# Kernel optimization log

Hardware: AMD Instinct MI355X
Metric: run time of the kernel (lower is better)

Reference implementation:

```python
import jax, jax.numpy as jnp
import numpy as np

EPS = 1e-10   # eps added inside cumprod, as in _compute_weights
FAR = 1e10    # last delta, as in forward()
NEAR_D, FAR_D = 2.0, 6.0  # typical NeRF near/far bounds for depth sampling

N_RAYS, N_PTS = 65536, 128


def setup_inputs() -> dict:
    key = jax.random.key(0)
    k1, k2, k3 = jax.random.split(key, 3)
    # densities are non-negative (raw sigma output after relu/softplus)
    density = jax.random.uniform(k1, (N_RAYS, N_PTS), dtype=jnp.float32) * 2.0
    feature = jax.random.uniform(k2, (N_RAYS, N_PTS, 3), dtype=jnp.float32)
    # monotonically increasing sample depths along each ray in [NEAR_D, FAR_D]
    depth_values = jnp.sort(
        jax.random.uniform(k3, (N_RAYS, N_PTS), dtype=jnp.float32,
                           minval=NEAR_D, maxval=FAR_D), axis=-1)
    return {"density": density, "feature": feature, "depth_values": depth_values}


def reference(density, feature, depth_values):
    # deltas: diff of sample depths, last delta = 1e10  -> [N, P]
    deltas = jnp.concatenate(
        [depth_values[..., 1:] - depth_values[..., :-1],
         jnp.full_like(depth_values[..., :1], FAR)], axis=-1)
    alpha = 1.0 - jnp.exp(-deltas * density)                      # [N, P]
    # transmittance: cumprod(1-alpha+eps) rolled right with T[...,0]=1
    Tinc = jnp.cumprod(1.0 - alpha + EPS, axis=-1)                # [N, P]
    T = jnp.concatenate([jnp.ones_like(Tinc[..., :1]), Tinc[..., :-1]], axis=-1)
    weights = T * alpha                                           # [N, P]
    # weighted feature (rgb) and depth aggregation over samples
    rgb = jnp.einsum('np,npc->nc', weights, feature)              # [N, 3]
    depth = jnp.einsum('np,npc->nc', weights,
                       jnp.broadcast_to(depth_values[..., None], feature.shape))  # [N, 3]
    return rgb, depth
```

## Files before the change

kernel.cpp:

```cpp
#include <hip/hip_runtime.h>

#define N_PTS 128
#define EPS_F 1e-10f
#define FAR_F 1e10f

template<int CTRL, int ROW_MASK>
__device__ __forceinline__ float dpp_mov(float src, float old) {
    union { float f; int i; } s, o, r;
    s.f = src; o.f = old;
    r.i = __builtin_amdgcn_update_dpp(o.i, s.i, CTRL, ROW_MASK, 0xF, false);
    return r.f;
}

__device__ __forceinline__ float half32_reduce_add(float x) {
    x += dpp_mov<0x111, 0xF>(x, 0.0f);
    x += dpp_mov<0x112, 0xF>(x, 0.0f);
    x += dpp_mov<0x114, 0xF>(x, 0.0f);
    x += dpp_mov<0x118, 0xF>(x, 0.0f);
    x += dpp_mov<0x142, 0xA>(x, 0.0f);
    return x;
}

__global__ __launch_bounds__(256) void volrend_kernel(
        const float* __restrict__ density,
        const float* __restrict__ feature,
        const float* __restrict__ depth,
        float* __restrict__ out, int n_rays) {
    const int lane = threadIdx.x & 63;
    const int hl   = lane & 31;
    const int wave = (blockIdx.x * 256 + threadIdx.x) >> 6;
    const int ray  = wave * 2 + (lane >> 5);

    const float4 dns = ((const float4*)(density + (size_t)ray * N_PTS))[hl];
    const float4 z   = ((const float4*)(depth   + (size_t)ray * N_PTS))[hl];
    const float4* fp = (const float4*)(feature + (size_t)ray * (N_PTS * 3));
    const float4 fa = fp[hl * 3 + 0];
    const float4 fb = fp[hl * 3 + 1];
    const float4 fc = fp[hl * 3 + 2];

    float nz = dpp_mov<0x130, 0xF>(z.x, 0.0f);
    float d0 = z.y - z.x;
    float d1 = z.z - z.y;
    float d2 = z.w - z.z;
    float d3 = (hl == 31) ? FAR_F : (nz - z.w);

    float e0 = __expf(-d0 * dns.x), e1 = __expf(-d1 * dns.y);
    float e2 = __expf(-d2 * dns.z), e3 = __expf(-d3 * dns.w);
    float f0 = e0 + EPS_F, f1 = e1 + EPS_F, f2 = e2 + EPS_F, f3 = e3 + EPS_F;
    float a0 = 1.0f - e0,  a1 = 1.0f - e1,  a2 = 1.0f - e2,  a3 = 1.0f - e3;

    float p = (f0 * f1) * (f2 * f3);
    p *= dpp_mov<0x111, 0xF>(p, 1.0f);
    p *= dpp_mov<0x112, 0xF>(p, 1.0f);
    p *= dpp_mov<0x114, 0xF>(p, 1.0f);
    p *= dpp_mov<0x118, 0xF>(p, 1.0f);
    p *= dpp_mov<0x142, 0xA>(p, 1.0f);
    float T0 = dpp_mov<0x138, 0xF>(p, 1.0f);
    T0 = (hl == 0) ? 1.0f : T0;

    float w0 = T0 * a0; float T1 = T0 * f0;
    float w1 = T1 * a1; float T2 = T1 * f1;
    float w2 = T2 * a2; float T3 = T2 * f2;
    float w3 = T3 * a3;

    float rx = half32_reduce_add(w0 * fa.x + w1 * fa.w + w2 * fb.z + w3 * fc.y);
    float ry = half32_reduce_add(w0 * fa.y + w1 * fb.x + w2 * fb.w + w3 * fc.z);
    float rz = half32_reduce_add(w0 * fa.z + w1 * fb.y + w2 * fc.x + w3 * fc.w);
    float dd = half32_reduce_add(w0 * z.x  + w1 * z.y  + w2 * z.z  + w3 * z.w);

    if (hl == 31) {
        float* o  = out + (size_t)ray * 3;
        o[0] = rx; o[1] = ry; o[2] = rz;
        float* od = out + (size_t)n_rays * 3 + (size_t)ray * 3;
        od[0] = dd; od[1] = dd; od[2] = dd;
    }
}

extern "C" void kernel_launch(void* const* d_in, const int* in_sizes, int n_in,
                              void* d_out, int out_size, void* d_ws, size_t ws_size,
                              hipStream_t stream) {
    const float* density = (const float*)d_in[0];
    const float* feature = (const float*)d_in[1];
    const float* depth   = (const float*)d_in[2];
    float* out = (float*)d_out;
    const int n_rays = in_sizes[0] / N_PTS;
    const int blocks = (n_rays + 7) / 8;
    volrend_kernel<<<blocks, 256, 0, stream>>>(density, feature, depth, out, n_rays);
}
```

Before: 191.2 us.

## Use persistent grid-stride loop with register prefetch of next ray pair

Measured after the change: 194.9 us. About the same (+2.0%).

```diff
diff --git a/kernel.cpp b/kernel.cpp
--- a/kernel.cpp
+++ b/kernel.cpp
@@ -28,51 +28,78 @@
         float* __restrict__ out, int n_rays) {
     const int lane = threadIdx.x & 63;
     const int hl   = lane & 31;
-    const int wave = (blockIdx.x * 256 + threadIdx.x) >> 6;
-    const int ray  = wave * 2 + (lane >> 5);
+    const int half = lane >> 5;
+    const int wave0  = (blockIdx.x * blockDim.x + threadIdx.x) >> 6;
+    const int nwaves = (gridDim.x * blockDim.x) >> 6;
+    const int npairs = n_rays >> 1;
 
-    const float4 dns = ((const float4*)(density + (size_t)ray * N_PTS))[hl];
-    const float4 z   = ((const float4*)(depth   + (size_t)ray * N_PTS))[hl];
-    const float4* fp = (const float4*)(feature + (size_t)ray * (N_PTS * 3));
-    const float4 fa = fp[hl * 3 + 0];
-    const float4 fb = fp[hl * 3 + 1];
-    const float4 fc = fp[hl * 3 + 2];
+    int p = wave0;
+    if (p >= npairs) return;
 
-    float nz = dpp_mov<0x130, 0xF>(z.x, 0.0f);
-    float d0 = z.y - z.x;
-    float d1 = z.z - z.y;
-    float d2 = z.w - z.z;
-    float d3 = (hl == 31) ? FAR_F : (nz - z.w);
+    int ray = p * 2 + half;
+    float4 dns = ((const float4*)(density + (size_t)ray * N_PTS))[hl];
+    float4 z   = ((const float4*)(depth   + (size_t)ray * N_PTS))[hl];
+    const float4* fp0 = (const float4*)(feature + (size_t)ray * (N_PTS * 3));
+    float4 fa = fp0[hl * 3 + 0];
+    float4 fb = fp0[hl * 3 + 1];
+    float4 fc = fp0[hl * 3 + 2];
 
-    float e0 = __expf(-d0 * dns.x), e1 = __expf(-d1 * dns.y);
-    float e2 = __expf(-d2 * dns.z), e3 = __expf(-d3 * dns.w);
-    float f0 = e0 + EPS_F, f1 = e1 + EPS_F, f2 = e2 + EPS_F, f3 = e3 + EPS_F;
-    float a0 = 1.0f - e0,  a1 = 1.0f - e1,  a2 = 1.0f - e2,  a3 = 1.0f - e3;
+    while (true) {
+        const int pn = p + nwaves;
+        const bool have_next = (pn < npairs);
 
-    float p = (f0 * f1) * (f2 * f3);
-    p *= dpp_mov<0x111, 0xF>(p, 1.0f);
-    p *= dpp_mov<0x112, 0xF>(p, 1.0f);
-    p *= dpp_mov<0x114, 0xF>(p, 1.0f);
-    p *= dpp_mov<0x118, 0xF>(p, 1.0f);
-    p *= dpp_mov<0x142, 0xA>(p, 1.0f);
-    float T0 = dpp_mov<0x138, 0xF>(p, 1.0f);
-    T0 = (hl == 0) ? 1.0f : T0;
+        float4 dns2, z2, fa2, fb2, fc2;
+        if (have_next) {
+            const int rayn = pn * 2 + half;
+            dns2 = ((const float4*)(density + (size_t)rayn * N_PTS))[hl];
+            z2   = ((const float4*)(depth   + (size_t)rayn * N_PTS))[hl];
+            const float4* fpn = (const float4*)(feature + (size_t)rayn * (N_PTS * 3));
+            fa2 = fpn[hl * 3 + 0];
+            fb2 = fpn[hl * 3 + 1];
+            fc2 = fpn[hl * 3 + 2];
+        }
 
-    float w0 = T0 * a0; float T1 = T0 * f0;
-    float w1 = T1 * a1; float T2 = T1 * f1;
-    float w2 = T2 * a2; float T3 = T2 * f2;
-    float w3 = T3 * a3;
+        float nz = dpp_mov<0x130, 0xF>(z.x, 0.0f);
+        float d0 = z.y - z.x;
+        float d1 = z.z - z.y;
+        float d2 = z.w - z.z;
+        float d3 = (hl == 31) ? FAR_F : (nz - z.w);
 
-    float rx = half32_reduce_add(w0 * fa.x + w1 * fa.w + w2 * fb.z + w3 * fc.y);
-    float ry = half32_reduce_add(w0 * fa.y + w1 * fb.x + w2 * fb.w + w3 * fc.z);
-    float rz = half32_reduce_add(w0 * fa.z + w1 * fb.y + w2 * fc.x + w3 * fc.w);
-    float dd = half32_reduce_add(w0 * z.x  + w1 * z.y  + w2 * z.z  + w3 * z.w);
+        float e0 = __expf(-d0 * dns.x), e1 = __expf(-d1 * dns.y);
+        float e2 = __expf(-d2 * dns.z), e3 = __expf(-d3 * dns.w);
+        float f0 = e0 + EPS_F, f1 = e1 + EPS_F, f2 = e2 + EPS_F, f3 = e3 + EPS_F;
+        float a0 = 1.0f - e0,  a1 = 1.0f - e1,  a2 = 1.0f - e2,  a3 = 1.0f - e3;
 
-    if (hl == 31) {
-        float* o  = out + (size_t)ray * 3;
-        o[0] = rx; o[1] = ry; o[2] = rz;
-        float* od = out + (size_t)n_rays * 3 + (size_t)ray * 3;
-        od[0] = dd; od[1] = dd; od[2] = dd;
+        float pr = (f0 * f1) * (f2 * f3);
+        pr *= dpp_mov<0x111, 0xF>(pr, 1.0f);
+        pr *= dpp_mov<0x112, 0xF>(pr, 1.0f);
+        pr *= dpp_mov<0x114, 0xF>(pr, 1.0f);
+        pr *= dpp_mov<0x118, 0xF>(pr, 1.0f);
+        pr *= dpp_mov<0x142, 0xA>(pr, 1.0f);
+        float T0 = dpp_mov<0x138, 0xF>(pr, 1.0f);
+        T0 = (hl == 0) ? 1.0f : T0;
+
+        float w0 = T0 * a0; float T1 = T0 * f0;
+        float w1 = T1 * a1; float T2 = T1 * f1;
+        float w2 = T2 * a2; float T3 = T2 * f2;
+        float w3 = T3 * a3;
+
+        float rx = half32_reduce_add(w0 * fa.x + w1 * fa.w + w2 * fb.z + w3 * fc.y);
+        float ry = half32_reduce_add(w0 * fa.y + w1 * fb.x + w2 * fb.w + w3 * fc.z);
+        float rz = half32_reduce_add(w0 * fa.z + w1 * fb.y + w2 * fc.x + w3 * fc.w);
+        float dd = half32_reduce_add(w0 * z.x  + w1 * z.y  + w2 * z.z  + w3 * z.w);
+
+        if (hl == 31) {
+            float* o  = out + (size_t)ray * 3;
+            o[0] = rx; o[1] = ry; o[2] = rz;
+            float* od = out + (size_t)n_rays * 3 + (size_t)ray * 3;
+            od[0] = dd; od[1] = dd; od[2] = dd;
+        }
+
+        if (!have_next) break;
+        p   = pn;
+        ray = p * 2 + half;
+        dns = dns2; z = z2; fa = fa2; fb = fb2; fc = fc2;
     }
 }
 
@@ -84,6 +111,6 @@
     const float* depth   = (const float*)d_in[2];
     float* out = (float*)d_out;
     const int n_rays = in_sizes[0] / N_PTS;
-    const int blocks = (n_rays + 7) / 8;
+    const int blocks = 1024;
     volrend_kernel<<<blocks, 256, 0, stream>>>(density, feature, depth, out, n_rays);
 }
```
